# Kernel tuning notes

Measured on AMD Instinct MI355X. Metric: run time of the kernel, lower is better.

The kernel has to match this reference:

```python
import jax, jax.numpy as jnp
import numpy as np

N = 100000        # nodes
E = 1600000       # edges (avg degree 16)
D_IN = 128
HIDDEN = (128, 128)
NS = 0.5          # leaky_relu negative slope


def _glorot(k, shape):
    lim = (6.0 / (shape[0] + shape[1])) ** 0.5
    return jax.random.uniform(k, shape, jnp.float32, -lim, lim)


def setup_inputs() -> dict:
    key = jax.random.key(0)
    ks = jax.random.split(key, 6)
    x = jax.random.normal(ks[0], (N, D_IN), dtype=jnp.float32)
    edge_index = jax.random.randint(ks[1], (2, E), 0, N, dtype=jnp.int32)
    # SAGEConv layer 1: lin_l (on aggregated neighbors, carries bias), lin_r (root)
    W1_l = _glorot(ks[2], (HIDDEN[0], D_IN))
    W1_r = _glorot(ks[3], (HIDDEN[0], D_IN))
    b1 = jnp.zeros((HIDDEN[0],), jnp.float32)
    # SAGEConv layer 2
    W2_l = _glorot(ks[4], (HIDDEN[1], HIDDEN[0]))
    W2_r = _glorot(ks[5], (HIDDEN[1], HIDDEN[0]))
    b2 = jnp.zeros((HIDDEN[1],), jnp.float32)
    return {"x": x, "edge_index": edge_index,
            "W1_l": W1_l, "W1_r": W1_r, "b1": b1,
            "W2_l": W2_l, "W2_r": W2_r, "b2": b2}


def _sage_layer(h, src, dst, deg_inv, W_l, W_r, b):
    # mean-aggregate neighbor features per target node, then linear + root linear + bias
    agg = jax.ops.segment_sum(h[src], dst, num_segments=N) * deg_inv  # [N, d_in]
    return agg @ W_l.T + h @ W_r.T + b


def reference(x, edge_index, W1_l, W1_r, b1, W2_l, W2_r, b2):
    src, dst = edge_index[0], edge_index[1]
    deg = jax.ops.segment_sum(jnp.ones((E,), x.dtype), dst, num_segments=N)
    deg_inv = (1.0 / jnp.maximum(deg, 1.0))[:, None]  # mean aggr; avoid div-by-zero
    # dropout is identity in eval mode; layer = SAGEConv -> leaky_relu(ns)
    h = jax.nn.leaky_relu(_sage_layer(x, src, dst, deg_inv, W1_l, W1_r, b1), NS)
    h = jax.nn.leaky_relu(_sage_layer(h, src, dst, deg_inv, W2_l, W2_r, b2), NS)
    return h
```

## Files before the change

### kernel.cpp

```cpp
#include <hip/hip_runtime.h>
#include <hip/hip_bf16.h>

#define NN 100000
#define NE 1600000
#define D  128
#define NB 196
#define BSLOT 10240
#define BCHUNK 8192

typedef short bf16x8 __attribute__((ext_vector_type(8)));
typedef float f32x4 __attribute__((ext_vector_type(4)));

static __device__ inline unsigned short f2b(float f) {
    __hip_bfloat16 b = __float2bfloat16(f);
    unsigned short u;
    __builtin_memcpy(&u, &b, 2);
    return u;
}

__global__ __launch_bounds__(1024) void bin_scatter(const int* __restrict__ ei,
                                                    int* __restrict__ gcur,
                                                    unsigned* __restrict__ ebuf) {
    __shared__ int hist[NB];
    __shared__ int base_s[NB];
    int chunk0 = blockIdx.x * BCHUNK;
    for (int t = threadIdx.x; t < NB; t += 1024) hist[t] = 0;
    __syncthreads();
    for (int i = 0; i < BCHUNK; i += 1024) {
        int e = chunk0 + i + threadIdx.x;
        if (e < NE) atomicAdd(&hist[ei[NE + e] >> 9], 1);
    }
    __syncthreads();
    for (int t = threadIdx.x; t < NB; t += 1024) {
        base_s[t] = hist[t] ? atomicAdd(&gcur[t], hist[t]) : 0;
        hist[t] = 0;
    }
    __syncthreads();
    for (int i = 0; i < BCHUNK; i += 1024) {
        int e = chunk0 + i + threadIdx.x;
        if (e < NE) {
            int s = ei[e];
            int d = ei[NE + e];
            int b = d >> 9;
            int off = atomicAdd(&hist[b], 1);
            ebuf[(size_t)base_s[b] + off] = ((unsigned)(d & 511) << 17) | (unsigned)s;
        }
    }
}

__global__ __launch_bounds__(512) void sort_bucket(
    const unsigned* __restrict__ ebuf, const int* __restrict__ gcur,
    int* __restrict__ rowbeg, int* __restrict__ rowend, int* __restrict__ col)
{
    __shared__ int cnt[512];
    __shared__ int tmp[512];
    __shared__ int cur[512];
    const int b = blockIdx.x;
    const int t = threadIdx.x;
    const int beg = b * BSLOT;
    const int end = gcur[b];
    const int node0 = b << 9;

    cnt[t] = 0;
    __syncthreads();
    for (int j = beg + t; j < end; j += 512)
        atomicAdd(&cnt[ebuf[j] >> 17], 1);
    __syncthreads();

    int v = cnt[t];
    tmp[t] = v;
    __syncthreads();
    for (int off = 1; off < 512; off <<= 1) {
        int tv = (t >= off) ? tmp[t - off] : 0;
        __syncthreads();
        tmp[t] += tv;
        __syncthreads();
    }
    int gpos = beg + (tmp[t] - v);
    if (node0 + t < NN) { rowbeg[node0 + t] = gpos; rowend[node0 + t] = gpos + v; }
    cur[t] = gpos;
    __syncthreads();

    for (int j = beg + t; j < end; j += 512) {
        unsigned p = ebuf[j];
        int pos = atomicAdd(&cur[p >> 17], 1);
        col[pos] = (int)(p & 0x1ffffu);
    }
}

__global__ void conv_all(const float* __restrict__ x,
                         const float* __restrict__ s0, const float* __restrict__ s1,
                         const float* __restrict__ s2, const float* __restrict__ s3,
                         unsigned short* __restrict__ xb,
                         unsigned short* __restrict__ wb,
                         int* __restrict__ gcur) {
    if (blockIdx.x == 0 && threadIdx.x < NB) gcur[threadIdx.x] = threadIdx.x * BSLOT;
    const int xn4 = NN * D / 4;
    int idx = blockIdx.x * 256 + threadIdx.x;
    if (idx < xn4) {
        int i = idx * 4;
        float4 v = *(const float4*)(x + i);
        ushort4 o;
        o.x = f2b(v.x); o.y = f2b(v.y); o.z = f2b(v.z); o.w = f2b(v.w);
        *(ushort4*)(xb + i) = o;
    } else if (idx < xn4 + 4 * D * D / 4) {
        int i = (idx - xn4) * 4;
        const float* srcs[4] = {s0, s1, s2, s3};
        int m = i >> 14;
        int rem = i & 16383;
        int j = rem >> 7, k = rem & 127;
        float4 v = *(const float4*)(srcs[m] + rem);
        ushort4 o;
        o.x = f2b(v.x); o.y = f2b(v.y); o.z = f2b(v.z); o.w = f2b(v.w);
        unsigned short* dst = wb + m * D * D
            + (((j >> 4) * 16 + (k >> 3)) * 16 + (j & 15)) * 8 + (k & 7);
        *(ushort4*)dst = o;
    }
}

__global__ __launch_bounds__(256) void aggregate(const unsigned short* __restrict__ hb,
                                                 const int* __restrict__ rowbeg,
                                                 const int* __restrict__ rowend,
                                                 const int* __restrict__ col,
                                                 unsigned short* __restrict__ aggb) {
    int node = blockIdx.x * 4 + (threadIdx.x >> 6);
    if (node >= NN) return;
    int lane = threadIdx.x & 63;
    int grp = lane >> 4;
    int gl  = lane & 15;
    int beg = rowbeg[node], end = rowend[node];
    const uint4* hp = (const uint4*)hb;
    float a0 = 0.f, a1 = 0.f, a2 = 0.f, a3 = 0.f;
    float a4 = 0.f, a5 = 0.f, a6 = 0.f, a7 = 0.f;

#define ACC8(V)                                                     \
    {                                                               \
        a0 += __uint_as_float((V).x << 16);                         \
        a1 += __uint_as_float((V).x & 0xffff0000u);                 \
        a2 += __uint_as_float((V).y << 16);                         \
        a3 += __uint_as_float((V).y & 0xffff0000u);                 \
        a4 += __uint_as_float((V).z << 16);                         \
        a5 += __uint_as_float((V).z & 0xffff0000u);                 \
        a6 += __uint_as_float((V).w << 16);                         \
        a7 += __uint_as_float((V).w & 0xffff0000u);                 \
    }

    int j = beg + grp;
    for (; j + 12 < end; j += 16) {
        int c0 = col[j];
        int c1 = col[j + 4];
        int c2 = col[j + 8];
        int c3 = col[j + 12];
        uint4 v0 = hp[(size_t)c0 * 16 + gl];
        uint4 v1 = hp[(size_t)c1 * 16 + gl];
        uint4 v2 = hp[(size_t)c2 * 16 + gl];
        uint4 v3 = hp[(size_t)c3 * 16 + gl];
        ACC8(v0); ACC8(v1); ACC8(v2); ACC8(v3);
    }
    for (; j < end; j += 4) {
        uint4 v = hp[(size_t)col[j] * 16 + gl];
        ACC8(v);
    }
#undef ACC8

#pragma unroll
    for (int off = 16; off < 64; off <<= 1) {
        a0 += __shfl_xor(a0, off);
        a1 += __shfl_xor(a1, off);
        a2 += __shfl_xor(a2, off);
        a3 += __shfl_xor(a3, off);
        a4 += __shfl_xor(a4, off);
        a5 += __shfl_xor(a5, off);
        a6 += __shfl_xor(a6, off);
        a7 += __shfl_xor(a7, off);
    }

    int deg = end - beg;
    float inv = 1.0f / (float)(deg > 1 ? deg : 1);
    if (grp == 0) {
        uint4 o;
        o.x = (unsigned)f2b(a0 * inv) | ((unsigned)f2b(a1 * inv) << 16);
        o.y = (unsigned)f2b(a2 * inv) | ((unsigned)f2b(a3 * inv) << 16);
        o.z = (unsigned)f2b(a4 * inv) | ((unsigned)f2b(a5 * inv) << 16);
        o.w = (unsigned)f2b(a6 * inv) | ((unsigned)f2b(a7 * inv) << 16);
        ((uint4*)aggb)[(size_t)node * 16 + gl] = o;
    }
}

template <int OUT_F32>
__global__ __launch_bounds__(256) void sage_gemm_mfma(
    const unsigned short* __restrict__ Ab,
    const unsigned short* __restrict__ Hb,
    const unsigned short* __restrict__ Wlb,
    const unsigned short* __restrict__ Wrb,
    const float* __restrict__ bias,
    float* __restrict__ outf,
    unsigned short* __restrict__ outb)
{
    __shared__ unsigned short sA[64][136];
    __shared__ unsigned short sH[64][136];
    const int tid = threadIdx.x;
    const int block0 = blockIdx.x * 64;

    {
        int i = tid;
#pragma unroll
        for (int k = 0; k < 4; ++k, i += 256) {
            int row = i >> 4, c16 = i & 15;
            int grow = block0 + row; if (grow >= NN) grow = NN - 1;
            *(uint4*)(&sA[row][c16 * 8]) = *(const uint4*)(Ab + (size_t)grow * D + c16 * 8);
            *(uint4*)(&sH[row][c16 * 8]) = *(const uint4*)(Hb + (size_t)grow * D + c16 * 8);
        }
    }
    __syncthreads();

    const int lane = tid & 63;
    const int wid  = tid >> 6;
    const int r  = lane & 15;
    const int kg = lane >> 4;
    const int rbase = (wid >> 1) * 32;
    const int col0  = (wid & 1) * 64;
    const int jb0   = col0 >> 4;

    float bv[4];
#pragma unroll
    for (int c = 0; c < 4; ++c) bv[c] = bias[col0 + c * 16 + r];

    f32x4 acc[2][4];
#pragma unroll
    for (int m = 0; m < 2; ++m)
#pragma unroll
        for (int c = 0; c < 4; ++c) acc[m][c] = (f32x4){0.f, 0.f, 0.f, 0.f};

#pragma unroll
    for (int ks = 0; ks < 8; ++ks) {
        const unsigned short (*S)[136] = (ks < 4) ? sA : sH;
        const unsigned short* W = (ks < 4) ? Wlb : Wrb;
        const int kk = (ks & 3) * 32 + kg * 8;
        const int kb = (ks & 3) * 4 + kg;
        bf16x8 a0 = *(const bf16x8*)(&S[rbase + r][kk]);
        bf16x8 a1 = *(const bf16x8*)(&S[rbase + 16 + r][kk]);
        bf16x8 bw[4];
#pragma unroll
        for (int c = 0; c < 4; ++c)
            bw[c] = *(const bf16x8*)(W + (((jb0 + c) * 16 + kb) * 16 + r) * 8);
#pragma unroll
        for (int c = 0; c < 4; ++c) {
            acc[0][c] = __builtin_amdgcn_mfma_f32_16x16x32_bf16(a0, bw[c], acc[0][c], 0, 0, 0);
            acc[1][c] = __builtin_amdgcn_mfma_f32_16x16x32_bf16(a1, bw[c], acc[1][c], 0, 0, 0);
        }
    }

#pragma unroll
    for (int m = 0; m < 2; ++m) {
#pragma unroll
        for (int q = 0; q < 4; ++q) {
            int row = block0 + rbase + m * 16 + kg * 4 + q;
            if (row < NN) {
#pragma unroll
                for (int c = 0; c < 4; ++c) {
                    float v = acc[m][c][q] + bv[c];
                    v = v > 0.f ? v : 0.5f * v;
                    int colj = col0 + c * 16 + r;
                    if (OUT_F32) outf[(size_t)row * D + colj] = v;
                    else         outb[(size_t)row * D + colj] = f2b(v);
                }
            }
        }
    }
}

extern "C" void kernel_launch(void* const* d_in, const int* in_sizes, int n_in,
                              void* d_out, int out_size, void* d_ws, size_t ws_size,
                              hipStream_t stream) {
    const float* x   = (const float*)d_in[0];
    const int*   ei  = (const int*)d_in[1];
    const float* W1l = (const float*)d_in[2];
    const float* W1r = (const float*)d_in[3];
    const float* b1  = (const float*)d_in[4];
    const float* W2l = (const float*)d_in[5];
    const float* W2r = (const float*)d_in[6];
    const float* b2  = (const float*)d_in[7];
    float* out = (float*)d_out;

    char* ws = (char*)d_ws;
    size_t off = 0;
    auto alloc = [&](size_t bytes) {
        void* p = ws + off;
        off = (off + bytes + 255) & ~(size_t)255;
        return p;
    };
    int* rowbeg = (int*)alloc((size_t)NN * 4);
    int* rowend = (int*)alloc((size_t)NN * 4);
    int* gcur   = (int*)alloc((NB + 1) * 4);
    int* col    = (int*)alloc((size_t)NB * BSLOT * 4);
    unsigned short* xb   = (unsigned short*)alloc((size_t)NN * D * 2);
    unsigned short* aggb = (unsigned short*)alloc((size_t)NN * D * 2);
    unsigned short* h1b  = (unsigned short*)alloc((size_t)NN * D * 2);
    unsigned short* wb   = (unsigned short*)alloc((size_t)4 * D * D * 2);
    unsigned short* w1lb = wb;
    unsigned short* w1rb = wb + D * D;
    unsigned short* w2lb = wb + 2 * D * D;
    unsigned short* w2rb = wb + 3 * D * D;
    unsigned* ebuf = (unsigned*)h1b;

    const int xn4 = NN * D / 4;
    conv_all<<<(xn4 + 4 * D * D / 4 + 255) / 256, 256, 0, stream>>>(
        x, W1l, W1r, W2l, W2r, xb, wb, gcur);

    bin_scatter<<<(NE + BCHUNK - 1) / BCHUNK, 1024, 0, stream>>>(ei, gcur, ebuf);
    sort_bucket<<<NB, 512, 0, stream>>>(ebuf, gcur, rowbeg, rowend, col);

    aggregate<<<(NN + 3) / 4, 256, 0, stream>>>(xb, rowbeg, rowend, col, aggb);
    sage_gemm_mfma<0><<<(NN + 63) / 64, 256, 0, stream>>>(aggb, xb, w1lb, w1rb, b1,
                                                          nullptr, h1b);
    aggregate<<<(NN + 3) / 4, 256, 0, stream>>>(h1b, rowbeg, rowend, col, aggb);
    sage_gemm_mfma<1><<<(NN + 63) / 64, 256, 0, stream>>>(aggb, h1b, w2lb, w2rb, b2,
                                                          out, nullptr);
}
```

Measured before the change: 212.9 us.

## Write aggregated features in MFMA fragment layout and load directly in GEMM

The aggregate kernel now processes 16 nodes per block (4 per wave) and stores its bf16 output in a blocked layout that matches the MFMA A-operand fragment order. The GEMM then reads the aggregated operand straight from global memory into registers, dropping the sA shared-memory tile and its staging stores. This cuts LDS traffic and occupancy pressure in the GEMM, but the aggregate store pattern becomes more scattered and each wave handles nodes serially, which may reduce latency hiding in the gather.

```diff
diff --git a/kernel.cpp b/kernel.cpp
--- a/kernel.cpp
+++ b/kernel.cpp
@@ -7,6 +7,7 @@
 #define NB 196
 #define BSLOT 10240
 #define BCHUNK 8192
+#define NBF (NN / 16)
 
 typedef short bf16x8 __attribute__((ext_vector_type(8)));
 typedef float f32x4 __attribute__((ext_vector_type(4)));
@@ -123,15 +124,19 @@
                                                  const int* __restrict__ rowend,
                                                  const int* __restrict__ col,
                                                  unsigned short* __restrict__ aggb) {
-    int node = blockIdx.x * 4 + (threadIdx.x >> 6);
-    if (node >= NN) return;
-    int lane = threadIdx.x & 63;
-    int grp = lane >> 4;
-    int gl  = lane & 15;
-    int beg = rowbeg[node], end = rowend[node];
+    const int nb = blockIdx.x;
+    const int node0 = nb * 16;
+    const int lane = threadIdx.x & 63;
+    const int w    = threadIdx.x >> 6;
+    const int grp = lane >> 4;
+    const int gl  = lane & 15;
     const uint4* hp = (const uint4*)hb;
-    float a0 = 0.f, a1 = 0.f, a2 = 0.f, a3 = 0.f;
-    float a4 = 0.f, a5 = 0.f, a6 = 0.f, a7 = 0.f;
+
+    for (int i = 0; i < 4; ++i) {
+        const int node = node0 + w * 4 + i;
+        const int beg = rowbeg[node], end = rowend[node];
+        float a0 = 0.f, a1 = 0.f, a2 = 0.f, a3 = 0.f;
+        float a4 = 0.f, a5 = 0.f, a6 = 0.f, a7 = 0.f;
 
 #define ACC8(V)                                                     \
     {                                                               \
@@ -144,46 +149,46 @@
         a6 += __uint_as_float((V).w << 16);                         \
         a7 += __uint_as_float((V).w & 0xffff0000u);                 \
     }
-
-    int j = beg + grp;
-    for (; j + 12 < end; j += 16) {
-        int c0 = col[j];
-        int c1 = col[j + 4];
-        int c2 = col[j + 8];
-        int c3 = col[j + 12];
-        uint4 v0 = hp[(size_t)c0 * 16 + gl];
-        uint4 v1 = hp[(size_t)c1 * 16 + gl];
-        uint4 v2 = hp[(size_t)c2 * 16 + gl];
-        uint4 v3 = hp[(size_t)c3 * 16 + gl];
-        ACC8(v0); ACC8(v1); ACC8(v2); ACC8(v3);
-    }
-    for (; j < end; j += 4) {
-        uint4 v = hp[(size_t)col[j] * 16 + gl];
-        ACC8(v);
-    }
+        int j = beg + grp;
+        for (; j + 12 < end; j += 16) {
+            int c0 = col[j];
+            int c1 = col[j + 4];
+            int c2 = col[j + 8];
+            int c3 = col[j + 12];
+            uint4 v0 = hp[(size_t)c0 * 16 + gl];
+            uint4 v1 = hp[(size_t)c1 * 16 + gl];
+            uint4 v2 = hp[(size_t)c2 * 16 + gl];
+            uint4 v3 = hp[(size_t)c3 * 16 + gl];
+            ACC8(v0); ACC8(v1); ACC8(v2); ACC8(v3);
+        }
+        for (; j < end; j += 4) {
+            uint4 v = hp[(size_t)col[j] * 16 + gl];
+            ACC8(v);
+        }
 #undef ACC8
 
 #pragma unroll
-    for (int off = 16; off < 64; off <<= 1) {
-        a0 += __shfl_xor(a0, off);
-        a1 += __shfl_xor(a1, off);
-        a2 += __shfl_xor(a2, off);
-        a3 += __shfl_xor(a3, off);
-        a4 += __shfl_xor(a4, off);
-        a5 += __shfl_xor(a5, off);
-        a6 += __shfl_xor(a6, off);
-        a7 += __shfl_xor(a7, off);
-    }
-
-    int deg = end - beg;
-    float inv = 1.0f / (float)(deg > 1 ? deg : 1);
-    if (grp == 0) {
-        uint4 o;
-        o.x = (unsigned)f2b(a0 * inv) | ((unsigned)f2b(a1 * inv) << 16);
-        o.y = (unsigned)f2b(a2 * inv) | ((unsigned)f2b(a3 * inv) << 16);
-        o.z = (unsigned)f2b(a4 * inv) | ((unsigned)f2b(a5 * inv) << 16);
-        o.w = (unsigned)f2b(a6 * inv) | ((unsigned)f2b(a7 * inv) << 16);
-        ((uint4*)aggb)[(size_t)node * 16 + gl] = o;
+        for (int off = 16; off < 64; off <<= 1) {
+            a0 += __shfl_xor(a0, off);
+            a1 += __shfl_xor(a1, off);
+            a2 += __shfl_xor(a2, off);
+            a3 += __shfl_xor(a3, off);
+            a4 += __shfl_xor(a4, off);
+            a5 += __shfl_xor(a5, off);
+            a6 += __shfl_xor(a6, off);
+            a7 += __shfl_xor(a7, off);
+        }
+
+        int deg = end - beg;
+        float inv = 1.0f / (float)(deg > 1 ? deg : 1);
+        if (grp == 0) {
+            uint4 o;
+            o.x = (unsigned)f2b(a0 * inv) | ((unsigned)f2b(a1 * inv) << 16);
+            o.y = (unsigned)f2b(a2 * inv) | ((unsigned)f2b(a3 * inv) << 16);
+            o.z = (unsigned)f2b(a4 * inv) | ((unsigned)f2b(a5 * inv) << 16);
+            o.w = (unsigned)f2b(a6 * inv) | ((unsigned)f2b(a7 * inv) << 16);
+            ((uint4*)aggb)[((size_t)nb * 16 + gl) * 16 + (node & 15)] = o;
+        }
     }
 }
 
@@ -197,7 +202,6 @@
     float* __restrict__ outf,
     unsigned short* __restrict__ outb)
 {
-    __shared__ unsigned short sA[64][136];
     __shared__ unsigned short sH[64][136];
     const int tid = threadIdx.x;
     const int block0 = blockIdx.x * 64;
@@ -208,7 +212,6 @@
         for (int k = 0; k < 4; ++k, i += 256) {
             int row = i >> 4, c16 = i & 15;
             int grow = block0 + row; if (grow >= NN) grow = NN - 1;
-            *(uint4*)(&sA[row][c16 * 8]) = *(const uint4*)(Ab + (size_t)grow * D + c16 * 8);
             *(uint4*)(&sH[row][c16 * 8]) = *(const uint4*)(Hb + (size_t)grow * D + c16 * 8);
         }
     }
@@ -221,6 +224,8 @@
     const int rbase = (wid >> 1) * 32;
     const int col0  = (wid & 1) * 64;
     const int jb0   = col0 >> 4;
+    const int nb0   = min((block0 + rbase) >> 4, NBF - 1);
+    const int nb1   = min(((block0 + rbase) >> 4) + 1, NBF - 1);
 
     float bv[4];
 #pragma unroll
@@ -234,12 +239,17 @@
 
 #pragma unroll
     for (int ks = 0; ks < 8; ++ks) {
-        const unsigned short (*S)[136] = (ks < 4) ? sA : sH;
+        const int kb = (ks & 3) * 4 + kg;
+        bf16x8 a0, a1;
+        if (ks < 4) {
+            a0 = *(const bf16x8*)(Ab + (((size_t)nb0 * 16 + kb) * 16 + r) * 8);
+            a1 = *(const bf16x8*)(Ab + (((size_t)nb1 * 16 + kb) * 16 + r) * 8);
+        } else {
+            const int kk = (ks & 3) * 32 + kg * 8;
+            a0 = *(const bf16x8*)(&sH[rbase + r][kk]);
+            a1 = *(const bf16x8*)(&sH[rbase + 16 + r][kk]);
+        }
         const unsigned short* W = (ks < 4) ? Wlb : Wrb;
-        const int kk = (ks & 3) * 32 + kg * 8;
-        const int kb = (ks & 3) * 4 + kg;
-        bf16x8 a0 = *(const bf16x8*)(&S[rbase + r][kk]);
-        bf16x8 a1 = *(const bf16x8*)(&S[rbase + 16 + r][kk]);
         bf16x8 bw[4];
 #pragma unroll
         for (int c = 0; c < 4; ++c)
@@ -311,10 +321,10 @@
     bin_scatter<<<(NE + BCHUNK - 1) / BCHUNK, 1024, 0, stream>>>(ei, gcur, ebuf);
     sort_bucket<<<NB, 512, 0, stream>>>(ebuf, gcur, rowbeg, rowend, col);
 
-    aggregate<<<(NN + 3) / 4, 256, 0, stream>>>(xb, rowbeg, rowend, col, aggb);
+    aggregate<<<NBF, 256, 0, stream>>>(xb, rowbeg, rowend, col, aggb);
     sage_gemm_mfma<0><<<(NN + 63) / 64, 256, 0, stream>>>(aggb, xb, w1lb, w1rb, b1,
                                                           nullptr, h1b);
-    aggregate<<<(NN + 3) / 4, 256, 0, stream>>>(h1b, rowbeg, rowend, col, aggb);
+    aggregate<<<NBF, 256, 0, stream>>>(h1b, rowbeg, rowend, col, aggb);
     sage_gemm_mfma<1><<<(NN + 63) / 64, 256, 0, stream>>>(aggb, h1b, w2lb, w2rb, b2,
                                                           out, nullptr);
 }
```

Result: slower. 249.9 us (+17.4%).
